# Kernel optimization log

Hardware: AMD Instinct MI355X
Metric: run time of the kernel (lower is better)

## Reference

```python
import jax, jax.numpy as jnp
import numpy as np

B, N, C_CLASS, C_CHARGE, S_MAX = 128, 256, 5, 3, 300


def setup_inputs() -> dict:
    key = jax.random.key(0)
    ks = jax.random.split(key, 12)
    return {
        "particle_class": jax.random.randint(ks[0], (B, N), 0, C_CLASS),
        "particle_charge": jax.random.randint(ks[1], (B, N), 0, C_CHARGE),
        "n_particles": jax.random.randint(ks[2], (B,), 0, S_MAX),
        "pflow_class_logits": jax.random.normal(ks[3], (B, N, C_CLASS), jnp.float32),
        "pflow_charge_logits": jax.random.normal(ks[4], (B, N, C_CHARGE), jnp.float32),
        "particle_pos": jax.random.normal(ks[5], (B, N, 3), jnp.float32),
        "pflow_pos": jax.random.normal(ks[6], (B, N, 3), jnp.float32),
        "particle_mom": jax.random.normal(ks[7], (B, N, 3), jnp.float32),
        "pflow_mom": jax.random.normal(ks[8], (B, N, 3), jnp.float32),
        "particle_energy": jax.random.normal(ks[9], (B, N), jnp.float32),
        "pflow_energy": jax.random.normal(ks[10], (B, N), jnp.float32),
        "predicted_setsizes": jax.random.normal(ks[11], (B, N, S_MAX), jnp.float32),
    }


def _pairwise_nll(logits, labels):
    # logits: [B, Nq, C] (pflow/dst side), labels: [B, Np] int (particle/src side)
    # returns CE(dst_logits_j, src_label_i) for every pair -> [B, Np, Nq]
    logp = jax.nn.log_softmax(logits, axis=-1)            # [B, Nq, C]
    idx = labels[:, :, None, None]                        # [B, Np, 1, 1]
    return -jnp.take_along_axis(logp[:, None, :, :], idx, axis=3)[..., 0]


def reference(particle_class, particle_charge, n_particles,
              pflow_class_logits, pflow_charge_logits,
              particle_pos, pflow_pos, particle_mom, pflow_mom,
              particle_energy, pflow_energy, predicted_setsizes):
    # per-edge (full bipartite per event) pair losses -> [B, Np, Nq]
    class_l = _pairwise_nll(pflow_class_logits, particle_class)
    charge_l = _pairwise_nll(pflow_charge_logits, particle_charge)
    pos_l = jnp.linalg.norm(particle_pos[:, :, None, :] - pflow_pos[:, None, :, :], axis=-1)
    mom_l = jnp.linalg.norm(particle_mom[:, :, None, :] - pflow_mom[:, None, :, :], axis=-1)
    en_l = (particle_energy[:, :, None] - pflow_energy[:, None, :]) ** 2
    pair_loss = class_l + charge_l + pos_l + mom_l + en_l  # [B, Np, Nq]

    # segment-min over mailbox: per-pflow min over incoming particle edges,
    # per-particle min over incoming pflow edges
    min_per_pflow = pair_loss.min(axis=1)      # [B, Nq]
    min_per_particle = pair_loss.min(axis=2)   # [B, Np]

    particle_loss = min_per_particle.sum(axis=1).mean()
    pflow_loss = min_per_pflow.sum(axis=1).mean()

    # setsize: mean over pflow nodes per event, CE against true multiplicity
    setsize_logp = jax.nn.log_softmax(predicted_setsizes.mean(axis=1), axis=-1)  # [B, S]
    setsize_loss = -jnp.take_along_axis(setsize_logp, n_particles[:, None], axis=1)[:, 0].mean()

    loss = particle_loss + pflow_loss + setsize_loss
    return loss
```

## Files before the change

### kernel.cpp

```cpp
#include <hip/hip_runtime.h>
#include <math.h>

#define BQ 128
#define NQ 256
#define SMAX 300
#define CCLS 5
#define CCHG 3
#define TSTR 268
#define RSTR 12
#define INFV 3.0e38f

#define NPAIR 256
#define NMAIN (NPAIR + BQ)

__device__ __forceinline__ float fast_sqrtf(float x) {
    return __builtin_amdgcn_sqrtf(x);
}

#define P_TAB   0
#define P_COLS  4020
#define P_ROWS  6068
#define P_RED   7604
#define P_PART  9652
#define SMEM_FLOATS 9656


__global__ __launch_bounds__(512, 2) void main_kernel(
    const int* __restrict__ p_class, const int* __restrict__ p_charge,
    const int* __restrict__ n_particles,
    const float* __restrict__ cls_logits, const float* __restrict__ chg_logits,
    const float* __restrict__ p_pos, const float* __restrict__ pf_pos,
    const float* __restrict__ p_mom, const float* __restrict__ pf_mom,
    const float* __restrict__ p_en, const float* __restrict__ pf_en,
    const float* __restrict__ setsizes, float* __restrict__ ws,
    float* __restrict__ out)
{
    __shared__ float smem[SMEM_FLOATS];
    const int t = threadIdx.x;
    const int blk = blockIdx.x;

    if (blk < NPAIR) {
        const int b  = blk >> 1;
        const int rh = blk & 1;
        const int base = b * NQ;
        float* s_tab  = smem + P_TAB;
        float* s_cols = smem + P_COLS;
        float* s_rows = smem + P_ROWS;
        float* s_red  = smem + P_RED;
        float* s_part = smem + P_PART;

        if (t < NQ) {
            const int gj = base + t;
            const float* cl = cls_logits + (size_t)gj * CCLS;
            float l0=cl[0], l1=cl[1], l2=cl[2], l3=cl[3], l4=cl[4];
            float mx = fmaxf(fmaxf(fmaxf(l0,l1),fmaxf(l2,l3)),l4);
            float lse = mx + __logf(__expf(l0-mx)+__expf(l1-mx)+__expf(l2-mx)+
                                    __expf(l3-mx)+__expf(l4-mx));
            const float* gl = chg_logits + (size_t)gj * CCHG;
            float g0=gl[0], g1=gl[1], g2=gl[2];
            float gmx = fmaxf(fmaxf(g0,g1),g2);
            float glse = gmx + __logf(__expf(g0-gmx)+__expf(g1-gmx)+__expf(g2-gmx));
            float nc[CCLS] = {lse-l0, lse-l1, lse-l2, lse-l3, lse-l4};
            float ng[CCHG] = {glse-g0, glse-g1, glse-g2};
            #pragma unroll
            for (int c = 0; c < CCLS; ++c)
                #pragma unroll
                for (int g = 0; g < CCHG; ++g)
                    s_tab[(c*CCHG+g)*TSTR + t] = nc[c] + ng[g];

            float* cr = &s_cols[t*8];
            cr[0]=pf_pos[gj*3+0]; cr[1]=pf_pos[gj*3+1]; cr[2]=pf_pos[gj*3+2];
            cr[3]=pf_mom[gj*3+0]; cr[4]=pf_mom[gj*3+1]; cr[5]=pf_mom[gj*3+2];
            cr[6]=pf_en[gj];      cr[7]=0.0f;
        } else if (t < NQ + 128) {
            const int rr = t - NQ;
            const int gr = base + rh*128 + rr;
            float* rw = &s_rows[rr*RSTR];
            rw[0]=p_pos[gr*3+0]; rw[1]=p_pos[gr*3+1]; rw[2]=p_pos[gr*3+2];
            rw[3]=p_mom[gr*3+0]; rw[4]=p_mom[gr*3+1]; rw[5]=p_mom[gr*3+2];
            rw[6]=p_en[gr];
            rw[7]=__int_as_float(p_class[gr]*CCHG + p_charge[gr]);
        }
        __syncthreads();

        const int tx = t & 31;
        const int ty = t >> 5;
        const int c0 = ty * 16;

        float4 ra[4], rb[4];
        int ccr[4];
        #pragma unroll
        for (int r = 0; r < 4; ++r) {
            const int row = tx + 32*r;
            ra[r] = *(const float4*)&s_rows[row*RSTR];
            rb[r] = *(const float4*)&s_rows[row*RSTR + 4];
            ccr[r] = __float_as_int(rb[r].w) * TSTR;
        }
        float cmin[16];
        #pragma unroll
        for (int c = 0; c < 16; ++c) cmin[c] = INFV;
        float rmin[4] = {INFV, INFV, INFV, INFV};

        #pragma unroll 4
        for (int c = 0; c < 16; ++c) {
            const int j = c0 + c;
            const float4 cd0 = *(const float4*)&s_cols[j*8];
            const float4 cd1 = *(const float4*)&s_cols[j*8+4];
            float cm = cmin[c];
            #pragma unroll
            for (int r = 0; r < 4; ++r) {
                float dx=ra[r].x-cd0.x, dy=ra[r].y-cd0.y, dz=ra[r].z-cd0.z;
                float ex=ra[r].w-cd0.w, ey=rb[r].x-cd1.x, ez=rb[r].y-cd1.y;
                float de=rb[r].z-cd1.z;
                float v = s_tab[ccr[r] + j]
                        + fast_sqrtf(dx*dx + dy*dy + dz*dz)
                        + fast_sqrtf(ex*ex + ey*ey + ez*ez)
                        + de*de;
                rmin[r] = fminf(rmin[r], v);
                cm = fminf(cm, v);
            }
            cmin[c] = cm;
        }

        #pragma unroll 4
        for (int c = 0; c < 16; ++c) {
            float v = cmin[c];
            #pragma unroll
            for (int off = 16; off > 0; off >>= 1)
                v = fminf(v, __shfl_down(v, off, 32));
            if (tx == 0) ws[blk*NQ + c0 + c] = v;
        }
        #pragma unroll
        for (int r = 0; r < 4; ++r)
            s_red[ty*128 + tx + 32*r] = rmin[r];
        __syncthreads();

        if (t < 128) {
            float m = s_red[t];
            #pragma unroll
            for (int k = 1; k < 16; ++k) m = fminf(m, s_red[k*128 + t]);
            #pragma unroll
            for (int off = 32; off > 0; off >>= 1) m += __shfl_down(m, off, 64);
            if ((t & 63) == 0) s_part[t >> 6] = m;
        }
        __syncthreads();
        if (t == 0)
            atomicAdd(out, (s_part[0] + s_part[1]) * (1.0f / BQ));

    } else {
        const int b = blk - NPAIR;
        float* s_ss = smem;
        float* s_m  = smem + 608;
        float* s_p5 = smem + 912;
        float* s_one= smem + 920;

        const int slice = t >> 8;
        const int col = t & 255;
        const float* bp = setsizes + (size_t)b * NQ * SMAX + (size_t)(slice*128) * SMAX;
        {
            const float* p = bp + col;
            float acc = 0.f;
            #pragma unroll 16
            for (int i = 0; i < 128; ++i) acc += p[(size_t)i * SMAX];
            s_ss[slice*304 + col] = acc;
        }
        if (col < SMAX - NQ) {
            const float* p = bp + (NQ + col);
            float acc = 0.f;
            #pragma unroll 16
            for (int i = 0; i < 128; ++i) acc += p[(size_t)i * SMAX];
            s_ss[slice*304 + NQ + col] = acc;
        }
        __syncthreads();
        float m = -INFV;
        if (t < SMAX) { m = (s_ss[t] + s_ss[304 + t]) * (1.0f / NQ); s_m[t] = m; }
        const int wave = t >> 6, lane = t & 63;
        float wm = m;
        #pragma unroll
        for (int off = 32; off > 0; off >>= 1) wm = fmaxf(wm, __shfl_down(wm, off));
        if (lane == 0 && wave < 5) s_p5[wave] = wm;
        __syncthreads();
        if (t == 0)
            s_one[0] = fmaxf(fmaxf(fmaxf(s_p5[0], s_p5[1]), fmaxf(s_p5[2], s_p5[3])), s_p5[4]);
        __syncthreads();
        const float mx = s_one[0];
        float e = (t < SMAX) ? __expf(m - mx) : 0.f;
        #pragma unroll
        for (int off = 32; off > 0; off >>= 1) e += __shfl_down(e, off);
        if (lane == 0 && wave < 5) s_p5[wave] = e;
        __syncthreads();
        if (t == 0) {
            float s = s_p5[0] + s_p5[1] + s_p5[2] + s_p5[3] + s_p5[4];
            int nb = n_particles[b];
            float loss = -(s_m[nb] - mx - __logf(s));
            atomicAdd(out, loss * (1.0f / BQ));
        }
    }
}

__global__ __launch_bounds__(256) void finish_kernel(
    const float* __restrict__ ws, float* __restrict__ out)
{
    const int b = blockIdx.x;
    const int t = threadIdx.x;
    __shared__ float s_p[4];
    float v = fminf(ws[(b*2)*NQ + t], ws[(b*2+1)*NQ + t]);
    #pragma unroll
    for (int off = 32; off > 0; off >>= 1) v += __shfl_down(v, off, 64);
    if ((t & 63) == 0) s_p[t >> 6] = v;
    __syncthreads();
    if (t == 0)
        atomicAdd(out, (s_p[0] + s_p[1] + s_p[2] + s_p[3]) * (1.0f / BQ));
}

extern "C" void kernel_launch(void* const* d_in, const int* in_sizes, int n_in,
                              void* d_out, int out_size, void* d_ws, size_t ws_size,
                              hipStream_t stream) {
    (void)in_sizes; (void)n_in; (void)ws_size;
    const int*   p_class     = (const int*)d_in[0];
    const int*   p_charge    = (const int*)d_in[1];
    const int*   n_particles = (const int*)d_in[2];
    const float* cls_logits  = (const float*)d_in[3];
    const float* chg_logits  = (const float*)d_in[4];
    const float* p_pos       = (const float*)d_in[5];
    const float* pf_pos      = (const float*)d_in[6];
    const float* p_mom       = (const float*)d_in[7];
    const float* pf_mom      = (const float*)d_in[8];
    const float* p_en        = (const float*)d_in[9];
    const float* pf_en       = (const float*)d_in[10];
    const float* setsizes    = (const float*)d_in[11];
    float* out = (float*)d_out;
    float* ws  = (float*)d_ws;

    (void)hipMemsetAsync(out, 0, sizeof(float) * (size_t)out_size, stream);

    main_kernel<<<NMAIN, 512, 0, stream>>>(
        p_class, p_charge, n_particles, cls_logits, chg_logits,
        p_pos, pf_pos, p_mom, pf_mom, p_en, pf_en, setsizes, ws, out);

    finish_kernel<<<BQ, 256, 0, stream>>>(ws, out);
}
```

Before: 117.4 us.

## Process whole event per block and fuse column-min finish into main kernel

Each pair block now handles one full event, looping over both 128-row halves, instead of two blocks per event. Column minima therefore stay in registers across the halves and are reduced and summed in-kernel, which removes the workspace writes and the separate finish kernel launch. The cost is half as many pair blocks (128 rather than 256) with twice the serial work each. That lowers parallelism on a GPU with many CUs and leaves the pair blocks sharing the grid with the setsize blocks. The memset is also capped to a small size.

```diff
diff --git a/kernel.cpp b/kernel.cpp
--- a/kernel.cpp
+++ b/kernel.cpp
@@ -10,7 +10,7 @@
 #define RSTR 12
 #define INFV 3.0e38f
 
-#define NPAIR 256
+#define NPAIR 128
 #define NMAIN (NPAIR + BQ)
 
 __device__ __forceinline__ float fast_sqrtf(float x) {
@@ -20,10 +20,9 @@
 #define P_TAB   0
 #define P_COLS  4020
 #define P_ROWS  6068
-#define P_RED   7604
-#define P_PART  9652
-#define SMEM_FLOATS 9656
-
+#define P_RED   9140
+#define P_PART  11188
+#define SMEM_FLOATS 11212
 
 __global__ __launch_bounds__(512, 2) void main_kernel(
     const int* __restrict__ p_class, const int* __restrict__ p_charge,
@@ -32,16 +31,14 @@
     const float* __restrict__ p_pos, const float* __restrict__ pf_pos,
     const float* __restrict__ p_mom, const float* __restrict__ pf_mom,
     const float* __restrict__ p_en, const float* __restrict__ pf_en,
-    const float* __restrict__ setsizes, float* __restrict__ ws,
-    float* __restrict__ out)
+    const float* __restrict__ setsizes, float* __restrict__ out)
 {
     __shared__ float smem[SMEM_FLOATS];
     const int t = threadIdx.x;
     const int blk = blockIdx.x;
 
     if (blk < NPAIR) {
-        const int b  = blk >> 1;
-        const int rh = blk & 1;
+        const int b    = blk;
         const int base = b * NQ;
         float* s_tab  = smem + P_TAB;
         float* s_cols = smem + P_COLS;
@@ -72,9 +69,9 @@
             cr[0]=pf_pos[gj*3+0]; cr[1]=pf_pos[gj*3+1]; cr[2]=pf_pos[gj*3+2];
             cr[3]=pf_mom[gj*3+0]; cr[4]=pf_mom[gj*3+1]; cr[5]=pf_mom[gj*3+2];
             cr[6]=pf_en[gj];      cr[7]=0.0f;
-        } else if (t < NQ + 128) {
+        } else {
             const int rr = t - NQ;
-            const int gr = base + rh*128 + rr;
+            const int gr = base + rr;
             float* rw = &s_rows[rr*RSTR];
             rw[0]=p_pos[gr*3+0]; rw[1]=p_pos[gr*3+1]; rw[2]=p_pos[gr*3+2];
             rw[3]=p_mom[gr*3+0]; rw[4]=p_mom[gr*3+1]; rw[5]=p_mom[gr*3+2];
@@ -87,65 +84,77 @@
         const int ty = t >> 5;
         const int c0 = ty * 16;
 
-        float4 ra[4], rb[4];
-        int ccr[4];
-        #pragma unroll
-        for (int r = 0; r < 4; ++r) {
-            const int row = tx + 32*r;
-            ra[r] = *(const float4*)&s_rows[row*RSTR];
-            rb[r] = *(const float4*)&s_rows[row*RSTR + 4];
-            ccr[r] = __float_as_int(rb[r].w) * TSTR;
-        }
         float cmin[16];
         #pragma unroll
         for (int c = 0; c < 16; ++c) cmin[c] = INFV;
-        float rmin[4] = {INFV, INFV, INFV, INFV};
-
-        #pragma unroll 4
-        for (int c = 0; c < 16; ++c) {
-            const int j = c0 + c;
-            const float4 cd0 = *(const float4*)&s_cols[j*8];
-            const float4 cd1 = *(const float4*)&s_cols[j*8+4];
-            float cm = cmin[c];
+
+        #pragma unroll 1
+        for (int rh = 0; rh < 2; ++rh) {
+            float4 ra[4], rb[4];
+            int ccr[4];
             #pragma unroll
             for (int r = 0; r < 4; ++r) {
-                float dx=ra[r].x-cd0.x, dy=ra[r].y-cd0.y, dz=ra[r].z-cd0.z;
-                float ex=ra[r].w-cd0.w, ey=rb[r].x-cd1.x, ez=rb[r].y-cd1.y;
-                float de=rb[r].z-cd1.z;
-                float v = s_tab[ccr[r] + j]
-                        + fast_sqrtf(dx*dx + dy*dy + dz*dz)
-                        + fast_sqrtf(ex*ex + ey*ey + ez*ez)
-                        + de*de;
-                rmin[r] = fminf(rmin[r], v);
-                cm = fminf(cm, v);
+                const int row = rh*128 + tx + 32*r;
+                ra[r] = *(const float4*)&s_rows[row*RSTR];
+                rb[r] = *(const float4*)&s_rows[row*RSTR + 4];
+                ccr[r] = __float_as_int(rb[r].w) * TSTR;
             }
-            cmin[c] = cm;
-        }
-
-        #pragma unroll 4
+            float rmin[4] = {INFV, INFV, INFV, INFV};
+
+            #pragma unroll 4
+            for (int c = 0; c < 16; ++c) {
+                const int j = c0 + c;
+                const float4 cd0 = *(const float4*)&s_cols[j*8];
+                const float4 cd1 = *(const float4*)&s_cols[j*8+4];
+                float cm = cmin[c];
+                #pragma unroll
+                for (int r = 0; r < 4; ++r) {
+                    float dx=ra[r].x-cd0.x, dy=ra[r].y-cd0.y, dz=ra[r].z-cd0.z;
+                    float ex=ra[r].w-cd0.w, ey=rb[r].x-cd1.x, ez=rb[r].y-cd1.y;
+                    float de=rb[r].z-cd1.z;
+                    float v = s_tab[ccr[r] + j]
+                            + fast_sqrtf(dx*dx + dy*dy + dz*dz)
+                            + fast_sqrtf(ex*ex + ey*ey + ez*ez)
+                            + de*de;
+                    rmin[r] = fminf(rmin[r], v);
+                    cm = fminf(cm, v);
+                }
+                cmin[c] = cm;
+            }
+
+            #pragma unroll
+            for (int r = 0; r < 4; ++r)
+                s_red[ty*128 + tx + 32*r] = rmin[r];
+            __syncthreads();
+            if (t < 128) {
+                float m = s_red[t];
+                #pragma unroll
+                for (int k = 1; k < 16; ++k) m = fminf(m, s_red[k*128 + t]);
+                #pragma unroll
+                for (int off = 32; off > 0; off >>= 1) m += __shfl_down(m, off, 64);
+                if ((t & 63) == 0) s_part[20 + rh*2 + (t >> 6)] = m;
+            }
+            __syncthreads();
+        }
+
+        float colsum = 0.0f;
+        #pragma unroll
         for (int c = 0; c < 16; ++c) {
             float v = cmin[c];
             #pragma unroll
             for (int off = 16; off > 0; off >>= 1)
                 v = fminf(v, __shfl_down(v, off, 32));
-            if (tx == 0) ws[blk*NQ + c0 + c] = v;
-        }
-        #pragma unroll
-        for (int r = 0; r < 4; ++r)
-            s_red[ty*128 + tx + 32*r] = rmin[r];
-        __syncthreads();
-
-        if (t < 128) {
-            float m = s_red[t];
-            #pragma unroll
-            for (int k = 1; k < 16; ++k) m = fminf(m, s_red[k*128 + t]);
-            #pragma unroll
-            for (int off = 32; off > 0; off >>= 1) m += __shfl_down(m, off, 64);
-            if ((t & 63) == 0) s_part[t >> 6] = m;
-        }
-        __syncthreads();
-        if (t == 0)
-            atomicAdd(out, (s_part[0] + s_part[1]) * (1.0f / BQ));
+            colsum += v;
+        }
+        if (tx == 0) s_part[ty] = colsum;
+        __syncthreads();
+        if (t == 0) {
+            float cs = 0.0f;
+            #pragma unroll
+            for (int k = 0; k < 16; ++k) cs += s_part[k];
+            float rs = s_part[20] + s_part[21] + s_part[22] + s_part[23];
+            atomicAdd(out, (cs + rs) * (1.0f / BQ));
+        }
 
     } else {
         const int b = blk - NPAIR;
@@ -198,25 +207,10 @@
     }
 }
 
-__global__ __launch_bounds__(256) void finish_kernel(
-    const float* __restrict__ ws, float* __restrict__ out)
-{
-    const int b = blockIdx.x;
-    const int t = threadIdx.x;
-    __shared__ float s_p[4];
-    float v = fminf(ws[(b*2)*NQ + t], ws[(b*2+1)*NQ + t]);
-    #pragma unroll
-    for (int off = 32; off > 0; off >>= 1) v += __shfl_down(v, off, 64);
-    if ((t & 63) == 0) s_p[t >> 6] = v;
-    __syncthreads();
-    if (t == 0)
-        atomicAdd(out, (s_p[0] + s_p[1] + s_p[2] + s_p[3]) * (1.0f / BQ));
-}
-
 extern "C" void kernel_launch(void* const* d_in, const int* in_sizes, int n_in,
                               void* d_out, int out_size, void* d_ws, size_t ws_size,
                               hipStream_t stream) {
-    (void)in_sizes; (void)n_in; (void)ws_size;
+    (void)in_sizes; (void)n_in; (void)d_ws; (void)ws_size;
     const int*   p_class     = (const int*)d_in[0];
     const int*   p_charge    = (const int*)d_in[1];
     const int*   n_particles = (const int*)d_in[2];
@@ -230,13 +224,12 @@
     const float* pf_en       = (const float*)d_in[10];
     const float* setsizes    = (const float*)d_in[11];
     float* out = (float*)d_out;
-    float* ws  = (float*)d_ws;
-
-    (void)hipMemsetAsync(out, 0, sizeof(float) * (size_t)out_size, stream);
+
+    size_t zb = (size_t)out_size * sizeof(float);
+    if (zb > 4096) zb = 4096;
+    (void)hipMemsetAsync(out, 0, zb, stream);
 
     main_kernel<<<NMAIN, 512, 0, stream>>>(
         p_class, p_charge, n_particles, cls_logits, chg_logits,
-        p_pos, pf_pos, p_mom, pf_mom, p_en, pf_en, setsizes, ws, out);
-
-    finish_kernel<<<BQ, 256, 0, stream>>>(ws, out);
+        p_pos, pf_pos, p_mom, pf_mom, p_en, pf_en, setsizes, out);
 }
```

Result: faster. 108.8 us, median of 2 (-7.4%).

## Interleave setsize streaming into pair blocks and replace atomics with deterministic reduction

Applied to the files above, without the earlier changes.

Removes the separate setsize blocks and has each pair block stream its half-event slice of predicted_setsizes in chunks, interleaved with the pairwise min computation, so memory loads overlap ALU work. Partial results go to workspace instead of atomics. A combine kernel computes per-event losses, and a single-block final kernel writes the output, which replaces the memset. This adds a third launch and more register pressure from the 32-value load buffer under launch_bounds(512,2).

```diff
diff --git a/kernel.cpp b/kernel.cpp
--- a/kernel.cpp
+++ b/kernel.cpp
@@ -10,12 +10,12 @@
 #define RSTR 12
 #define INFV 3.0e38f
 
-#define NPAIR 256
-#define NMAIN (NPAIR + BQ)
-
-__device__ __forceinline__ float fast_sqrtf(float x) {
-    return __builtin_amdgcn_sqrtf(x);
-}
+#define NBLK 256
+
+#define W_COL 0
+#define W_SC  65536
+#define W_SS  65792
+#define W_B   143616
 
 #define P_TAB   0
 #define P_COLS  4020
@@ -24,89 +24,99 @@
 #define P_PART  9652
 #define SMEM_FLOATS 9656
 
+__device__ __forceinline__ float fast_sqrtf(float x) {
+    return __builtin_amdgcn_sqrtf(x);
+}
 
 __global__ __launch_bounds__(512, 2) void main_kernel(
     const int* __restrict__ p_class, const int* __restrict__ p_charge,
-    const int* __restrict__ n_particles,
     const float* __restrict__ cls_logits, const float* __restrict__ chg_logits,
     const float* __restrict__ p_pos, const float* __restrict__ pf_pos,
     const float* __restrict__ p_mom, const float* __restrict__ pf_mom,
     const float* __restrict__ p_en, const float* __restrict__ pf_en,
-    const float* __restrict__ setsizes, float* __restrict__ ws,
-    float* __restrict__ out)
+    const float* __restrict__ setsizes, float* __restrict__ ws)
 {
     __shared__ float smem[SMEM_FLOATS];
-    const int t = threadIdx.x;
+    const int t   = threadIdx.x;
     const int blk = blockIdx.x;
-
-    if (blk < NPAIR) {
-        const int b  = blk >> 1;
-        const int rh = blk & 1;
-        const int base = b * NQ;
-        float* s_tab  = smem + P_TAB;
-        float* s_cols = smem + P_COLS;
-        float* s_rows = smem + P_ROWS;
-        float* s_red  = smem + P_RED;
-        float* s_part = smem + P_PART;
-
-        if (t < NQ) {
-            const int gj = base + t;
-            const float* cl = cls_logits + (size_t)gj * CCLS;
-            float l0=cl[0], l1=cl[1], l2=cl[2], l3=cl[3], l4=cl[4];
-            float mx = fmaxf(fmaxf(fmaxf(l0,l1),fmaxf(l2,l3)),l4);
-            float lse = mx + __logf(__expf(l0-mx)+__expf(l1-mx)+__expf(l2-mx)+
-                                    __expf(l3-mx)+__expf(l4-mx));
-            const float* gl = chg_logits + (size_t)gj * CCHG;
-            float g0=gl[0], g1=gl[1], g2=gl[2];
-            float gmx = fmaxf(fmaxf(g0,g1),g2);
-            float glse = gmx + __logf(__expf(g0-gmx)+__expf(g1-gmx)+__expf(g2-gmx));
-            float nc[CCLS] = {lse-l0, lse-l1, lse-l2, lse-l3, lse-l4};
-            float ng[CCHG] = {glse-g0, glse-g1, glse-g2};
-            #pragma unroll
-            for (int c = 0; c < CCLS; ++c)
-                #pragma unroll
-                for (int g = 0; g < CCHG; ++g)
-                    s_tab[(c*CCHG+g)*TSTR + t] = nc[c] + ng[g];
-
-            float* cr = &s_cols[t*8];
-            cr[0]=pf_pos[gj*3+0]; cr[1]=pf_pos[gj*3+1]; cr[2]=pf_pos[gj*3+2];
-            cr[3]=pf_mom[gj*3+0]; cr[4]=pf_mom[gj*3+1]; cr[5]=pf_mom[gj*3+2];
-            cr[6]=pf_en[gj];      cr[7]=0.0f;
-        } else if (t < NQ + 128) {
-            const int rr = t - NQ;
-            const int gr = base + rh*128 + rr;
-            float* rw = &s_rows[rr*RSTR];
-            rw[0]=p_pos[gr*3+0]; rw[1]=p_pos[gr*3+1]; rw[2]=p_pos[gr*3+2];
-            rw[3]=p_mom[gr*3+0]; rw[4]=p_mom[gr*3+1]; rw[5]=p_mom[gr*3+2];
-            rw[6]=p_en[gr];
-            rw[7]=__int_as_float(p_class[gr]*CCHG + p_charge[gr]);
-        }
-        __syncthreads();
-
-        const int tx = t & 31;
-        const int ty = t >> 5;
-        const int c0 = ty * 16;
-
-        float4 ra[4], rb[4];
-        int ccr[4];
-        #pragma unroll
-        for (int r = 0; r < 4; ++r) {
-            const int row = tx + 32*r;
-            ra[r] = *(const float4*)&s_rows[row*RSTR];
-            rb[r] = *(const float4*)&s_rows[row*RSTR + 4];
-            ccr[r] = __float_as_int(rb[r].w) * TSTR;
-        }
-        float cmin[16];
-        #pragma unroll
-        for (int c = 0; c < 16; ++c) cmin[c] = INFV;
-        float rmin[4] = {INFV, INFV, INFV, INFV};
-
-        #pragma unroll 4
-        for (int c = 0; c < 16; ++c) {
-            const int j = c0 + c;
+    const int b   = blk >> 1;
+    const int h   = blk & 1;
+    const int base = b * NQ;
+
+    float* s_tab  = smem + P_TAB;
+    float* s_cols = smem + P_COLS;
+    float* s_rows = smem + P_ROWS;
+    float* s_red  = smem + P_RED;
+    float* s_part = smem + P_PART;
+
+    if (t < NQ) {
+        const int gj = base + t;
+        const float* cl = cls_logits + (size_t)gj * CCLS;
+        float l0=cl[0], l1=cl[1], l2=cl[2], l3=cl[3], l4=cl[4];
+        float mx = fmaxf(fmaxf(fmaxf(l0,l1),fmaxf(l2,l3)),l4);
+        float lse = mx + __logf(__expf(l0-mx)+__expf(l1-mx)+__expf(l2-mx)+
+                                __expf(l3-mx)+__expf(l4-mx));
+        const float* gl = chg_logits + (size_t)gj * CCHG;
+        float g0=gl[0], g1=gl[1], g2=gl[2];
+        float gmx = fmaxf(fmaxf(g0,g1),g2);
+        float glse = gmx + __logf(__expf(g0-gmx)+__expf(g1-gmx)+__expf(g2-gmx));
+        float nc[CCLS] = {lse-l0, lse-l1, lse-l2, lse-l3, lse-l4};
+        float ng[CCHG] = {glse-g0, glse-g1, glse-g2};
+        #pragma unroll
+        for (int c = 0; c < CCLS; ++c)
+            #pragma unroll
+            for (int g = 0; g < CCHG; ++g)
+                s_tab[(c*CCHG+g)*TSTR + t] = nc[c] + ng[g];
+
+        float* cr = &s_cols[t*8];
+        cr[0]=pf_pos[gj*3+0]; cr[1]=pf_pos[gj*3+1]; cr[2]=pf_pos[gj*3+2];
+        cr[3]=pf_mom[gj*3+0]; cr[4]=pf_mom[gj*3+1]; cr[5]=pf_mom[gj*3+2];
+        cr[6]=pf_en[gj];      cr[7]=0.0f;
+    } else if (t < NQ + 128) {
+        const int rr = t - NQ;
+        const int gr = base + h*128 + rr;
+        float* rw = &s_rows[rr*RSTR];
+        rw[0]=p_pos[gr*3+0]; rw[1]=p_pos[gr*3+1]; rw[2]=p_pos[gr*3+2];
+        rw[3]=p_mom[gr*3+0]; rw[4]=p_mom[gr*3+1]; rw[5]=p_mom[gr*3+2];
+        rw[6]=p_en[gr];
+        rw[7]=__int_as_float(p_class[gr]*CCHG + p_charge[gr]);
+    }
+    __syncthreads();
+
+    const int tx = t & 31;
+    const int ty = t >> 5;
+    const int c0 = ty * 16;
+
+    float4 ra[4], rb[4];
+    int ccr[4];
+    #pragma unroll
+    for (int r = 0; r < 4; ++r) {
+        const int row = tx + 32*r;
+        ra[r] = *(const float4*)&s_rows[row*RSTR];
+        rb[r] = *(const float4*)&s_rows[row*RSTR + 4];
+        ccr[r] = __float_as_int(rb[r].w) * TSTR;
+    }
+    float rmin[4] = {INFV, INFV, INFV, INFV};
+
+    const bool ssa = (t < SMAX);
+    const float* ssp = setsizes + ((size_t)base + (size_t)(h*128)) * SMAX + t;
+    float ssacc = 0.0f;
+
+    #pragma unroll 1
+    for (int chunk = 0; chunk < 4; ++chunk) {
+        float ssv[32];
+        if (ssa) {
+            #pragma unroll
+            for (int u = 0; u < 32; ++u)
+                ssv[u] = ssp[(size_t)(chunk*32 + u) * SMAX];
+        }
+
+        float cm[4] = {INFV, INFV, INFV, INFV};
+        #pragma unroll
+        for (int cc = 0; cc < 4; ++cc) {
+            const int j = c0 + chunk*4 + cc;
             const float4 cd0 = *(const float4*)&s_cols[j*8];
             const float4 cd1 = *(const float4*)&s_cols[j*8+4];
-            float cm = cmin[c];
             #pragma unroll
             for (int r = 0; r < 4; ++r) {
                 float dx=ra[r].x-cd0.x, dy=ra[r].y-cd0.y, dz=ra[r].z-cd0.z;
@@ -117,100 +127,102 @@
                         + fast_sqrtf(ex*ex + ey*ey + ez*ez)
                         + de*de;
                 rmin[r] = fminf(rmin[r], v);
-                cm = fminf(cm, v);
+                cm[cc]  = fminf(cm[cc], v);
             }
-            cmin[c] = cm;
-        }
-
-        #pragma unroll 4
-        for (int c = 0; c < 16; ++c) {
-            float v = cmin[c];
+        }
+
+        #pragma unroll
+        for (int cc = 0; cc < 4; ++cc) {
+            float v = cm[cc];
             #pragma unroll
             for (int off = 16; off > 0; off >>= 1)
                 v = fminf(v, __shfl_down(v, off, 32));
-            if (tx == 0) ws[blk*NQ + c0 + c] = v;
-        }
-        #pragma unroll
-        for (int r = 0; r < 4; ++r)
-            s_red[ty*128 + tx + 32*r] = rmin[r];
-        __syncthreads();
-
-        if (t < 128) {
-            float m = s_red[t];
-            #pragma unroll
-            for (int k = 1; k < 16; ++k) m = fminf(m, s_red[k*128 + t]);
-            #pragma unroll
-            for (int off = 32; off > 0; off >>= 1) m += __shfl_down(m, off, 64);
-            if ((t & 63) == 0) s_part[t >> 6] = m;
-        }
-        __syncthreads();
-        if (t == 0)
-            atomicAdd(out, (s_part[0] + s_part[1]) * (1.0f / BQ));
-
-    } else {
-        const int b = blk - NPAIR;
-        float* s_ss = smem;
-        float* s_m  = smem + 608;
-        float* s_p5 = smem + 912;
-        float* s_one= smem + 920;
-
-        const int slice = t >> 8;
-        const int col = t & 255;
-        const float* bp = setsizes + (size_t)b * NQ * SMAX + (size_t)(slice*128) * SMAX;
-        {
-            const float* p = bp + col;
-            float acc = 0.f;
-            #pragma unroll 16
-            for (int i = 0; i < 128; ++i) acc += p[(size_t)i * SMAX];
-            s_ss[slice*304 + col] = acc;
-        }
-        if (col < SMAX - NQ) {
-            const float* p = bp + (NQ + col);
-            float acc = 0.f;
-            #pragma unroll 16
-            for (int i = 0; i < 128; ++i) acc += p[(size_t)i * SMAX];
-            s_ss[slice*304 + NQ + col] = acc;
-        }
-        __syncthreads();
-        float m = -INFV;
-        if (t < SMAX) { m = (s_ss[t] + s_ss[304 + t]) * (1.0f / NQ); s_m[t] = m; }
-        const int wave = t >> 6, lane = t & 63;
-        float wm = m;
-        #pragma unroll
-        for (int off = 32; off > 0; off >>= 1) wm = fmaxf(wm, __shfl_down(wm, off));
-        if (lane == 0 && wave < 5) s_p5[wave] = wm;
-        __syncthreads();
-        if (t == 0)
-            s_one[0] = fmaxf(fmaxf(fmaxf(s_p5[0], s_p5[1]), fmaxf(s_p5[2], s_p5[3])), s_p5[4]);
-        __syncthreads();
-        const float mx = s_one[0];
-        float e = (t < SMAX) ? __expf(m - mx) : 0.f;
-        #pragma unroll
-        for (int off = 32; off > 0; off >>= 1) e += __shfl_down(e, off);
-        if (lane == 0 && wave < 5) s_p5[wave] = e;
-        __syncthreads();
-        if (t == 0) {
-            float s = s_p5[0] + s_p5[1] + s_p5[2] + s_p5[3] + s_p5[4];
-            int nb = n_particles[b];
-            float loss = -(s_m[nb] - mx - __logf(s));
-            atomicAdd(out, loss * (1.0f / BQ));
-        }
-    }
-}
-
-__global__ __launch_bounds__(256) void finish_kernel(
-    const float* __restrict__ ws, float* __restrict__ out)
+            if (tx == 0) ws[W_COL + blk*NQ + c0 + chunk*4 + cc] = v;
+        }
+
+        if (ssa) {
+            #pragma unroll
+            for (int u = 0; u < 32; ++u) ssacc += ssv[u];
+        }
+    }
+
+    if (ssa) ws[W_SS + blk*304 + t] = ssacc;
+
+    #pragma unroll
+    for (int r = 0; r < 4; ++r)
+        s_red[ty*128 + tx + 32*r] = rmin[r];
+    __syncthreads();
+    if (t < 128) {
+        float m = s_red[t];
+        #pragma unroll
+        for (int k = 1; k < 16; ++k) m = fminf(m, s_red[k*128 + t]);
+        #pragma unroll
+        for (int off = 32; off > 0; off >>= 1) m += __shfl_down(m, off, 64);
+        if ((t & 63) == 0) s_part[t >> 6] = m;
+    }
+    __syncthreads();
+    if (t == 0)
+        ws[W_SC + blk] = s_part[0] + s_part[1];
+}
+
+__global__ __launch_bounds__(512) void combine_kernel(
+    const int* __restrict__ n_particles, float* __restrict__ ws)
 {
+    __shared__ float s_p[8], s_q[8], s_m[304], s_one[1];
     const int b = blockIdx.x;
     const int t = threadIdx.x;
-    __shared__ float s_p[4];
-    float v = fminf(ws[(b*2)*NQ + t], ws[(b*2+1)*NQ + t]);
+    const int wave = t >> 6, lane = t & 63;
+
+    float v = 0.0f;
+    if (t < NQ)
+        v = fminf(ws[W_COL + (2*b)*NQ + t], ws[W_COL + (2*b+1)*NQ + t]);
     #pragma unroll
     for (int off = 32; off > 0; off >>= 1) v += __shfl_down(v, off, 64);
-    if ((t & 63) == 0) s_p[t >> 6] = v;
-    __syncthreads();
-    if (t == 0)
-        atomicAdd(out, (s_p[0] + s_p[1] + s_p[2] + s_p[3]) * (1.0f / BQ));
+    if (lane == 0) s_p[wave] = v;
+
+    float m = -INFV;
+    if (t < SMAX) {
+        m = (ws[W_SS + (2*b)*304 + t] + ws[W_SS + (2*b+1)*304 + t]) * (1.0f / NQ);
+        s_m[t] = m;
+    }
+    float wm = m;
+    #pragma unroll
+    for (int off = 32; off > 0; off >>= 1) wm = fmaxf(wm, __shfl_down(wm, off, 64));
+    if (lane == 0) s_q[wave] = wm;
+    __syncthreads();
+    if (t == 0) {
+        float a = fmaxf(fmaxf(s_q[0], s_q[1]), fmaxf(s_q[2], s_q[3]));
+        float c = fmaxf(fmaxf(s_q[4], s_q[5]), fmaxf(s_q[6], s_q[7]));
+        s_one[0] = fmaxf(a, c);
+    }
+    __syncthreads();
+    const float mx = s_one[0];
+    float e = (t < SMAX) ? __expf(m - mx) : 0.0f;
+    #pragma unroll
+    for (int off = 32; off > 0; off >>= 1) e += __shfl_down(e, off, 64);
+    if (lane == 0) s_q[wave] = e;
+    __syncthreads();
+    if (t == 0) {
+        float S = s_q[0]+s_q[1]+s_q[2]+s_q[3]+s_q[4]+s_q[5]+s_q[6]+s_q[7];
+        float colsum = s_p[0]+s_p[1]+s_p[2]+s_p[3]+s_p[4]+s_p[5]+s_p[6]+s_p[7];
+        int nb = n_particles[b];
+        float ssl = -(s_m[nb] - mx - __logf(S));
+        ws[W_B + b] = colsum + ws[W_SC + 2*b] + ws[W_SC + 2*b + 1] + ssl;
+    }
+}
+
+__global__ __launch_bounds__(128) void final_kernel(
+    const float* __restrict__ ws, float* __restrict__ out, int out_size)
+{
+    __shared__ float s2[2];
+    const int t = threadIdx.x;
+    float v = ws[W_B + t];
+    #pragma unroll
+    for (int off = 32; off > 0; off >>= 1) v += __shfl_down(v, off, 64);
+    if ((t & 63) == 0) s2[t >> 6] = v;
+    __syncthreads();
+    if (t == 0) out[0] = (s2[0] + s2[1]) * (1.0f / BQ);
+    for (int i = 1 + t; i < out_size && i < 1024; i += 128) out[i] = 0.0f;
 }
 
 extern "C" void kernel_launch(void* const* d_in, const int* in_sizes, int n_in,
@@ -232,11 +244,11 @@
     float* out = (float*)d_out;
     float* ws  = (float*)d_ws;
 
-    (void)hipMemsetAsync(out, 0, sizeof(float) * (size_t)out_size, stream);
-
-    main_kernel<<<NMAIN, 512, 0, stream>>>(
-        p_class, p_charge, n_particles, cls_logits, chg_logits,
-        p_pos, pf_pos, p_mom, pf_mom, p_en, pf_en, setsizes, ws, out);
-
-    finish_kernel<<<BQ, 256, 0, stream>>>(ws, out);
-}
+    main_kernel<<<NBLK, 512, 0, stream>>>(
+        p_class, p_charge, cls_logits, chg_logits,
+        p_pos, pf_pos, p_mom, pf_mom, p_en, pf_en, setsizes, ws);
+
+    combine_kernel<<<BQ, 512, 0, stream>>>(n_particles, ws);
+
+    final_kernel<<<1, 128, 0, stream>>>(ws, out, out_size);
+}
```

Result: faster. 109.9 us (-6.4%).
